# Kernel optimization log

Hardware: AMD Instinct MI355X
Metric: run time of the kernel (lower is better)

Reference implementation:

```python
import jax, jax.numpy as jnp
import numpy as np
from jax import lax

EPS = 0.1        # entropic regularization
MAX_ITER = 100   # Sinkhorn iteration budget
THRESH = 0.1     # early-stop threshold on err = mean_b sum_i |u - u_prev|
B, N, D = 16, 1024, 64


def setup_inputs() -> dict:
    key = jax.random.key(0)
    k1, k2 = jax.random.split(key)
    x = jax.random.normal(k1, (B, N, D), dtype=jnp.float32)
    y = jax.random.normal(k2, (B, N, D), dtype=jnp.float32)
    return {"x": x, "y": y}


def _lse(A):
    # Faithful to the original (unstabilized) lse: log(sum(exp(A)) + 1e-6)
    return jnp.log(jnp.exp(A).sum(-1) + 1e-6)


def _M(C, u, v):
    # (-C_ij + u_i + v_j) / eps
    return (-C + u[..., :, None] + v[..., None, :]) / EPS


def _cost_matrix(x, y):
    # (avoids materializing the [B, N, N, D] difference tensor; same math for p=2)
    x2 = (x * x).sum(-1)                         # [B, N]
    y2 = (y * y).sum(-1)                         # [B, N]
    xy = jnp.einsum('bid,bjd->bij', x, y)        # [B, N, N]
    return x2[..., :, None] + y2[..., None, :] - 2.0 * xy


def reference(x, y):
    x = jax.nn.softmax(x, axis=-1)
    y = jax.nn.softmax(y, axis=-1)
    C = _cost_matrix(x, y)                       # [B, N, N]
    n = x.shape[-2]
    log_mu = jnp.log(1.0 / n + 1e-8)             # mu = nu = uniform 1/n (scalar broadcast)
    u0 = jnp.zeros((x.shape[0], n), dtype=C.dtype)
    v0 = jnp.zeros_like(u0)

    def cond(carry):
        _, _, i, err = carry
        return jnp.logical_and(i < MAX_ITER, err >= THRESH)

    def body(carry):
        u, v, i, _ = carry
        u1 = u
        u = EPS * (log_mu - _lse(_M(C, u, v))) + u
        v = EPS * (log_mu - _lse(jnp.swapaxes(_M(C, u, v), -2, -1))) + v
        err = jnp.abs(u - u1).sum(-1).mean()
        return (u, v, i + 1, err)

    u, v, _, _ = lax.while_loop(
        cond, body, (u0, v0, jnp.int32(0), jnp.float32(jnp.inf)))

    pi = jnp.exp(_M(C, u, v))                    # transport plan [B, N, N]
    cost = (pi * C).sum((-2, -1))                # [B]
    return cost.mean()                           # reduction='mean'
```

## Files before the change

kernel.cpp:

```cpp
#include <hip/hip_runtime.h>
#include <hip/hip_bf16.h>
#include <math.h>

#define BATCH 16
#define NPTS 1024
#define DIM 64
#define EPSF 0.1f
#define INV_EPS 10.0f
#define MAX_ITER 100
#define THRESHF 0.1f
#define LSTRIDE 72

typedef _Float16 h8 __attribute__((ext_vector_type(8)));
typedef _Float16 half2v __attribute__((ext_vector_type(2)));
typedef short short8v __attribute__((ext_vector_type(8)));
typedef float float4v __attribute__((ext_vector_type(4)));

template <int P>
__device__ __forceinline__ half2v h2get(h8 v) {
  return __builtin_shufflevector(v, v, 2 * P, 2 * P + 1);
}

#define ATOMIC_ST(p, v) \
  __hip_atomic_store((p), (v), __ATOMIC_RELAXED, __HIP_MEMORY_SCOPE_AGENT)
#define ATOMIC_LD(p) \
  __hip_atomic_load((p), __ATOMIC_RELAXED, __HIP_MEMORY_SCOPE_AGENT)

__device__ inline float waveSum(float x) {
#pragma unroll
  for (int off = 32; off; off >>= 1) x += __shfl_xor(x, off, 64);
  return x;
}
__device__ inline float waveMax(float x) {
#pragma unroll
  for (int off = 32; off; off >>= 1) x = fmaxf(x, __shfl_xor(x, off, 64));
  return x;
}

__global__ __launch_bounds__(512, 2) void sinkhorn_fused(
    const float* __restrict__ x, const float* __restrict__ y,
    __hip_bfloat16* __restrict__ syh,
    float* __restrict__ y2,
    float* __restrict__ colsum,
    long long* __restrict__ flags,
    float* __restrict__ errB,
    float* __restrict__ costPart,
    float* __restrict__ out) {
  __shared__ __attribute__((aligned(16))) short xs[64 * LSTRIDE];
  __shared__ __attribute__((aligned(16))) short ys[2][64 * LSTRIDE];
  __shared__ __attribute__((aligned(16))) short os[2][64 * LSTRIDE];
  __shared__ __attribute__((aligned(16))) float wLDS[NPTS];
  __shared__ __attribute__((aligned(16))) _Float16 whL[NPTS];
  __shared__ __attribute__((aligned(16))) float colpart[8][NPTS];
  __shared__ float x2L[64];
  __shared__ float derr[8];
  __shared__ float errbL[BATCH];
  const int t = threadIdx.x;
  const int blk = blockIdx.x;
  const int wave = t >> 6, lane = t & 63;
  const int batch = (blk & 7) + 8 * (blk >> 7);
  const int kslot = (blk >> 3) & 15;
  const float log_mu = logf(1.0f / 1024.0f + 1e-8f);
  const float mu_c = 1.0f / 1024.0f + 1e-8f;

#pragma unroll
  for (int rr = 0; rr < 8; rr++) {
    int rl = wave * 8 + rr;
    int gr = batch * NPTS + kslot * 64 + rl;
    float xv = x[(size_t)gr * DIM + lane];
    float mx = waveMax(xv);
    float ex = __expf(xv - mx);
    float sx = waveSum(ex);
    float px = ex / sx;
    __hip_bfloat16 hbx = (__hip_bfloat16)px;
    xs[rl * LSTRIDE + lane] = *(const short*)&hbx;
    float sqx = waveSum(px * px);
    if (lane == 0) x2L[rl] = sqx;
    float yv = y[(size_t)gr * DIM + lane];
    float my = waveMax(yv);
    float ey = __expf(yv - my);
    float sy = waveSum(ey);
    float py = ey / sy;
    __hip_bfloat16 hby = (__hip_bfloat16)py;
    unsigned bits = *(const unsigned short*)&hby;
    unsigned nb = __shfl_down(bits, 1);
    if ((lane & 1) == 0)
      ATOMIC_ST((unsigned*)((unsigned short*)syh + (size_t)gr * DIM + lane),
                bits | (nb << 16));
    float sqy = waveSum(py * py);
    if (lane == 0) ATOMIC_ST(&y2[gr], sqy);
  }
  if (t < 192) {
    int buf = t >> 6, j = kslot * 64 + (t & 63);
    ATOMIC_ST(&colsum[((size_t)buf * BATCH + batch) * NPTS + j], 0.f);
  }
  __syncthreads();
  if (t == 0) ATOMIC_ST(&flags[batch * 16 + kslot], (long long)1 << 32);
  if (t < 16) {
    while ((int)(ATOMIC_LD(&flags[batch * 16 + t]) >> 32) < 1) {}
  }
  __syncthreads();

  const int m = lane & 15, q = lane >> 4;
  const int g = lane >> 3, sub = lane & 7;
  const int sw = wave & 3, ts = wave >> 2;
  short8v a0 = *(const short8v*)&xs[(sw * 16 + m) * LSTRIDE + q * 8];
  short8v a1 = *(const short8v*)&xs[(sw * 16 + m) * LSTRIDE + 32 + q * 8];
  float xa[4];
#pragma unroll
  for (int reg = 0; reg < 4; reg++) xa[reg] = x2L[sw * 16 + q * 4 + reg];
  h8 ka[8], kb[8];
  {
    const int r0 = t >> 3, c0 = (t & 7) * 8;
    const int r1 = (t + 512) >> 3, c1 = ((t + 512) & 7) * 8;
    const short* syb = (const short*)syh + (size_t)batch * NPTS * DIM;
    short8v pf0 = *(const short8v*)(syb + (size_t)r0 * DIM + c0);
    short8v pf1 = *(const short8v*)(syb + (size_t)r1 * DIM + c1);
    *(short8v*)&ys[r0 >> 6][(r0 & 63) * LSTRIDE + c0] = pf0;
    *(short8v*)&ys[r1 >> 6][(r1 & 63) * LSTRIDE + c1] = pf1;
    __syncthreads();
#pragma unroll
    for (int k = 0; k < 8; k++) {
      if (k < 7) {
        pf0 = *(const short8v*)(syb + (size_t)(128 * (k + 1) + r0) * DIM + c0);
        pf1 = *(const short8v*)(syb + (size_t)(128 * (k + 1) + r1) * DIM + c1);
      }
      const int jt = 2 * k + ts;
      float4v accv[4];
#pragma unroll
      for (int tj = 0; tj < 4; tj++) {
        short8v b0 = *(const short8v*)&ys[ts][(tj * 16 + m) * LSTRIDE + q * 8];
        short8v b1 = *(const short8v*)&ys[ts][(tj * 16 + m) * LSTRIDE + 32 + q * 8];
        float4v c = {0.f, 0.f, 0.f, 0.f};
        c = __builtin_amdgcn_mfma_f32_16x16x32_bf16(a0, b0, c, 0, 0, 0);
        c = __builtin_amdgcn_mfma_f32_16x16x32_bf16(a1, b1, c, 0, 0, 0);
        accv[tj] = c;
      }
#pragma unroll
      for (int tj = 0; tj < 4; tj++) {
        float y2v = y2[(size_t)batch * NPTS + jt * 64 + tj * 16 + m];
#pragma unroll
        for (int reg = 0; reg < 4; reg++) {
          float C = xa[reg] + y2v - 2.0f * accv[tj][reg];
          _Float16 kv = (_Float16)__expf(-INV_EPS * C);
          os[ts][(sw * 16 + q * 4 + reg) * LSTRIDE + tj * 16 + m] = *(const short*)&kv;
        }
      }
      __syncthreads();
      {
        int e0 = (2 * k) & 7, e1 = (2 * k + 1) & 7;
        if (g == e0 || g == e1) {
          const short* srcp = (g == e0) ? &os[0][0] : &os[1][0];
#pragma unroll
          for (int rr = 0; rr < 8; rr++) {
            h8 v = *(const h8*)&srcp[(wave * 8 + rr) * LSTRIDE + sub * 8];
            if (k < 4) ka[rr] = v; else kb[rr] = v;
          }
        }
      }
      if (k < 7) {
        *(short8v*)&ys[r0 >> 6][(r0 & 63) * LSTRIDE + c0] = pf0;
        *(short8v*)&ys[r1 >> 6][(r1 & 63) * LSTRIDE + c1] = pf1;
      }
      __syncthreads();
    }
  }

  for (int j = t; j < NPTS; j += 512) {
    wLDS[j] = 1.f;
    whL[j] = (_Float16)1.f;
  }
  __syncthreads();

  float eu[8], euPrev[8];
#pragma unroll
  for (int r = 0; r < 8; r++) eu[r] = 1.f;
  int it = 0;

  while (true) {
#pragma unroll
    for (int r = 0; r < 8; r++) euPrev[r] = eu[r];
    h8 wh0 = *(const h8*)&whL[8 * lane];
    h8 wh1 = *(const h8*)&whL[512 + 8 * lane];
    half2v c0[4], c1[4];
#pragma unroll
    for (int p = 0; p < 4; p++) {
      c0[p] = half2v{(_Float16)0.f, (_Float16)0.f};
      c1[p] = half2v{(_Float16)0.f, (_Float16)0.f};
    }
    float delta = 0.f;
#pragma unroll
    for (int rr = 0; rr < 8; rr++) {
      float d0 = 0.f, d1 = 0.f;
#define DOT_STEP(P)                                                         \
  d0 = __builtin_amdgcn_fdot2(h2get<P>(ka[rr]), h2get<P>(wh0), d0, false);  \
  d1 = __builtin_amdgcn_fdot2(h2get<P>(kb[rr]), h2get<P>(wh1), d1, false);
      DOT_STEP(0) DOT_STEP(1) DOT_STEP(2) DOT_STEP(3)
#undef DOT_STEP
      float dot = waveSum(d0 + d1);
      float sp = eu[rr] * dot + 1e-6f;
      float lg = __logf(sp);
      delta += fabsf(EPSF * (log_mu - lg));
      float ai = mu_c * eu[rr] * __builtin_amdgcn_rcpf(sp);
      eu[rr] = ai;
      _Float16 aih = (_Float16)(ai * 1024.0f);
      half2v ai2 = {aih, aih};
#define FMA_STEP(P)                                 \
  c0[P] = h2get<P>(ka[rr]) * ai2 + c0[P];           \
  c1[P] = h2get<P>(kb[rr]) * ai2 + c1[P];
      FMA_STEP(0) FMA_STEP(1) FMA_STEP(2) FMA_STEP(3)
#undef FMA_STEP
    }
    if (lane == 0) derr[wave] = delta;
    {
      float4* cp = (float4*)&colpart[wave][0];
      cp[2 * lane] = make_float4((float)c0[0][0], (float)c0[0][1],
                                 (float)c0[1][0], (float)c0[1][1]);
      cp[2 * lane + 1] = make_float4((float)c0[2][0], (float)c0[2][1],
                                     (float)c0[3][0], (float)c0[3][1]);
      cp[128 + 2 * lane] = make_float4((float)c1[0][0], (float)c1[0][1],
                                       (float)c1[1][0], (float)c1[1][1]);
      cp[128 + 2 * lane + 1] = make_float4((float)c1[2][0], (float)c1[2][1],
                                           (float)c1[3][0], (float)c1[3][1]);
    }
    __syncthreads();
    float* cs = colsum + ((size_t)(it % 3) * BATCH + batch) * NPTS;
    {
      int j0 = (t + (kslot << 6)) & 1023;
      int j1 = j0 ^ 512;
      float s0 = 0.f, s1 = 0.f;
#pragma unroll
      for (int w = 0; w < 8; w++) { s0 += colpart[w][j0]; s1 += colpart[w][j1]; }
      unsafeAtomicAdd(&cs[j0], s0);
      unsafeAtomicAdd(&cs[j1], s1);
    }
    if (it >= 1 && t < BATCH) {
      float v;
      while ((v = ATOMIC_LD(&errB[(it - 1) * BATCH + t])) < 0.f) {}
      errbL[t] = v;
    }
    float eblk = 0.f;
    if (t == 0) {
#pragma unroll
      for (int w = 0; w < 8; w++) eblk += derr[w];
    }
    __syncthreads();
    if (t == 0)
      ATOMIC_ST(&flags[batch * 16 + kslot],
                ((long long)(it + 2) << 32) | (long long)__float_as_uint(eblk));
    if (it >= 1) {
      float errv = 0.f;
#pragma unroll
      for (int k = 0; k < BATCH; k++) errv += errbL[k];
      if (errv * (1.0f / (float)BATCH) < THRESHF) {
#pragma unroll
        for (int r = 0; r < 8; r++) eu[r] = euPrev[r];
        break;
      }
    }
    float dpoll = 0.f;
    if (t < 16) {
      long long fw;
      while ((int)((fw = ATOMIC_LD(&flags[batch * 16 + t])) >> 32) < it + 2) {}
      dpoll = __uint_as_float((unsigned)fw);
    }
    __syncthreads();
    float cs0 = ATOMIC_LD(&cs[t]);
    float cs1 = ATOMIC_LD(&cs[t + 512]);
    if (t < 64)
      ATOMIC_ST(&colsum[((size_t)((it + 2) % 3) * BATCH + batch) * NPTS +
                        kslot * 64 + t], 0.f);
    if (wave == 0) {
      float e16 = (lane < 16) ? dpoll : 0.f;
#pragma unroll
      for (int off = 8; off; off >>= 1) e16 += __shfl_xor(e16, off, 16);
      if (t == 0 && kslot == 0) ATOMIC_ST(&errB[it * BATCH + batch], e16);
    }
    {
      float w0 = wLDS[t];
      float wn0 = mu_c * w0 *
                  __builtin_amdgcn_rcpf(w0 * cs0 + (1e-6f * 1024.0f)) * 1024.0f;
      wLDS[t] = wn0;
      whL[t] = (_Float16)wn0;
      float w1 = wLDS[t + 512];
      float wn1 = mu_c * w1 *
                  __builtin_amdgcn_rcpf(w1 * cs1 + (1e-6f * 1024.0f)) * 1024.0f;
      wLDS[t + 512] = wn1;
      whL[t + 512] = (_Float16)wn1;
    }
    it++;
    if (it >= MAX_ITER) break;
    __syncthreads();
  }

  {
    __syncthreads();
    const float4* w4 = (const float4*)wLDS;
    float wreg[16];
    *(float4*)&wreg[0]  = w4[2 * lane];
    *(float4*)&wreg[4]  = w4[2 * lane + 1];
    *(float4*)&wreg[8]  = w4[128 + 2 * lane];
    *(float4*)&wreg[12] = w4[128 + 2 * lane + 1];
    float csum = 0.f;
#pragma unroll
    for (int rr = 0; rr < 8; rr++) {
      float ai = eu[rr];
#pragma unroll
      for (int n = 0; n < 8; n++) {
        float kf = (float)ka[rr][n];
        if (kf > 0.f)
          csum += ai * wreg[n] * kf * (-EPSF * __logf(kf));
        float kg = (float)kb[rr][n];
        if (kg > 0.f)
          csum += ai * wreg[8 + n] * kg * (-EPSF * __logf(kg));
      }
    }
    csum = waveSum(csum);
    if (lane == 0) derr[wave] = csum;
    __syncthreads();
    if (t == 0) {
      float cst = 0.f;
#pragma unroll
      for (int w = 0; w < 8; w++) cst += derr[w];
      ATOMIC_ST(&costPart[blk], cst + 1.0f);
    }
    if (blk == 0) {
      if (t < 256) {
        float v;
        while ((v = ATOMIC_LD(&costPart[t])) < 0.5f) {}
        colpart[0][t] = v;
      }
      __syncthreads();
      if (wave == 0) {
        float s = colpart[0][lane] + colpart[0][lane + 64] +
                  colpart[0][lane + 128] + colpart[0][lane + 192];
        s = waveSum(s);
        if (lane == 0) out[0] = (s - 256.0f) * (1.0f / (float)BATCH);
      }
    }
  }
}

extern "C" void kernel_launch(void* const* d_in, const int* in_sizes, int n_in,
                              void* d_out, int out_size, void* d_ws,
                              size_t ws_size, hipStream_t stream) {
  (void)in_sizes; (void)n_in; (void)out_size; (void)ws_size;
  const float* x = (const float*)d_in[0];
  const float* y = (const float*)d_in[1];
  float* out = (float*)d_out;

  char* ws = (char*)d_ws;
  size_t off = 0;
  auto alloc = [&](size_t nbytes) -> void* {
    void* p = (void*)(ws + off);
    off = (off + nbytes + 255) & ~(size_t)255;
    return p;
  };
  __hip_bfloat16* syh = (__hip_bfloat16*)alloc((size_t)BATCH * NPTS * DIM * 2);
  float* y2 = (float*)alloc((size_t)BATCH * NPTS * 4);
  float* colsum = (float*)alloc((size_t)3 * BATCH * NPTS * 4);
  long long* flags = (long long*)alloc((size_t)BATCH * 16 * 8);
  float* errB = (float*)alloc((size_t)MAX_ITER * BATCH * 4);
  float* costPart = (float*)alloc(256 * 4);

  void* args[] = {&x, &y, &syh, &y2, &colsum, &flags,
                  &errB, &costPart, &out};
  hipLaunchCooperativeKernel((void*)sinkhorn_fused, dim3(256), dim3(512), args,
                             0, stream);
}
```

Before: 125.2 us.

## Pack two sub-blocks per 1024-thread workgroup with LDS-atomic group barriers

Runs two independent 512-thread slabs inside each 1024-thread workgroup, halving the cooperative grid to 128 blocks. Each slab synchronizes through its own LDS atomic-counter barrier with sleep polling, replacing __syncthreads. The per-wave column partials are also stored as fp16 instead of fp32 to shrink LDS. This trades hardware barriers for software spin barriers and reduces the precision of the partial sums. It also doubles LDS per block, which may limit residency.

After: 147.9 us. +18.2%, slower.

```diff
diff --git a/kernel.cpp b/kernel.cpp
--- a/kernel.cpp
+++ b/kernel.cpp
@@ -37,7 +37,21 @@
   return x;
 }
 
-__global__ __launch_bounds__(512, 2) void sinkhorn_fused(
+#define GBAR_IMPL(WAITSTR)                                                  \
+  do {                                                                      \
+    gen += 8;                                                               \
+    asm volatile(WAITSTR ::: "memory");                                     \
+    if (lane == 0)                                                          \
+      __hip_atomic_fetch_add(&bar[grp], 1, __ATOMIC_RELAXED,                \
+                             __HIP_MEMORY_SCOPE_WORKGROUP);                 \
+    while (__hip_atomic_load(&bar[grp], __ATOMIC_ACQUIRE,                   \
+                             __HIP_MEMORY_SCOPE_WORKGROUP) < gen)           \
+      __builtin_amdgcn_s_sleep(1);                                         \
+  } while (0)
+#define GBAR_L() GBAR_IMPL("s_waitcnt lgkmcnt(0)")
+#define GBAR_V() GBAR_IMPL("s_waitcnt vmcnt(0) lgkmcnt(0)")
+
+__global__ __launch_bounds__(1024, 4) void sinkhorn_fused(
     const float* __restrict__ x, const float* __restrict__ y,
     __hip_bfloat16* __restrict__ syh,
     float* __restrict__ y2,
@@ -46,22 +60,30 @@
     float* __restrict__ errB,
     float* __restrict__ costPart,
     float* __restrict__ out) {
-  __shared__ __attribute__((aligned(16))) short xs[64 * LSTRIDE];
-  __shared__ __attribute__((aligned(16))) short ys[2][64 * LSTRIDE];
-  __shared__ __attribute__((aligned(16))) short os[2][64 * LSTRIDE];
-  __shared__ __attribute__((aligned(16))) float wLDS[NPTS];
-  __shared__ __attribute__((aligned(16))) _Float16 whL[NPTS];
-  __shared__ __attribute__((aligned(16))) float colpart[8][NPTS];
-  __shared__ float x2L[64];
-  __shared__ float derr[8];
-  __shared__ float errbL[BATCH];
+  __shared__ __attribute__((aligned(16))) short xs[2][64 * LSTRIDE];
+  __shared__ __attribute__((aligned(16))) short ys[2][2][64 * LSTRIDE];
+  __shared__ __attribute__((aligned(16))) short os[2][2][64 * LSTRIDE];
+  __shared__ __attribute__((aligned(16))) float wLDS[2][NPTS];
+  __shared__ __attribute__((aligned(16))) _Float16 whL[2][NPTS];
+  __shared__ __attribute__((aligned(16))) _Float16 colpartH[2][8][NPTS];
+  __shared__ float x2L[2][64];
+  __shared__ float derrG[2][8];
+  __shared__ float errbL[2][BATCH];
+  __shared__ int bar[2];
   const int t = threadIdx.x;
-  const int blk = blockIdx.x;
-  const int wave = t >> 6, lane = t & 63;
-  const int batch = (blk & 7) + 8 * (blk >> 7);
-  const int kslot = (blk >> 3) & 15;
+  const int grp = t >> 9;
+  const int gt = t & 511;
+  const int wave = gt >> 6;
+  const int lane = t & 63;
+  const int sid = blockIdx.x * 2 + grp;
+  const int batch = (sid & 7) + 8 * (sid >> 7);
+  const int kslot = (sid >> 3) & 15;
   const float log_mu = logf(1.0f / 1024.0f + 1e-8f);
   const float mu_c = 1.0f / 1024.0f + 1e-8f;
+
+  if (t < 2) bar[t] = 0;
+  __syncthreads();
+  int gen = 0;
 
 #pragma unroll
   for (int rr = 0; rr < 8; rr++) {
@@ -73,9 +95,9 @@
     float sx = waveSum(ex);
     float px = ex / sx;
     __hip_bfloat16 hbx = (__hip_bfloat16)px;
-    xs[rl * LSTRIDE + lane] = *(const short*)&hbx;
+    xs[grp][rl * LSTRIDE + lane] = *(const short*)&hbx;
     float sqx = waveSum(px * px);
-    if (lane == 0) x2L[rl] = sqx;
+    if (lane == 0) x2L[grp][rl] = sqx;
     float yv = y[(size_t)gr * DIM + lane];
     float my = waveMax(yv);
     float ey = __expf(yv - my);
@@ -90,35 +112,35 @@
     float sqy = waveSum(py * py);
     if (lane == 0) ATOMIC_ST(&y2[gr], sqy);
   }
-  if (t < 192) {
-    int buf = t >> 6, j = kslot * 64 + (t & 63);
+  if (gt < 192) {
+    int buf = gt >> 6, j = kslot * 64 + (gt & 63);
     ATOMIC_ST(&colsum[((size_t)buf * BATCH + batch) * NPTS + j], 0.f);
   }
-  __syncthreads();
-  if (t == 0) ATOMIC_ST(&flags[batch * 16 + kslot], (long long)1 << 32);
-  if (t < 16) {
-    while ((int)(ATOMIC_LD(&flags[batch * 16 + t]) >> 32) < 1) {}
-  }
-  __syncthreads();
+  GBAR_V();
+  if (gt == 0) ATOMIC_ST(&flags[batch * 16 + kslot], (long long)1 << 32);
+  if (gt < 16) {
+    while ((int)(ATOMIC_LD(&flags[batch * 16 + gt]) >> 32) < 1) {}
+  }
+  GBAR_L();
 
   const int m = lane & 15, q = lane >> 4;
   const int g = lane >> 3, sub = lane & 7;
   const int sw = wave & 3, ts = wave >> 2;
-  short8v a0 = *(const short8v*)&xs[(sw * 16 + m) * LSTRIDE + q * 8];
-  short8v a1 = *(const short8v*)&xs[(sw * 16 + m) * LSTRIDE + 32 + q * 8];
+  short8v a0 = *(const short8v*)&xs[grp][(sw * 16 + m) * LSTRIDE + q * 8];
+  short8v a1 = *(const short8v*)&xs[grp][(sw * 16 + m) * LSTRIDE + 32 + q * 8];
   float xa[4];
 #pragma unroll
-  for (int reg = 0; reg < 4; reg++) xa[reg] = x2L[sw * 16 + q * 4 + reg];
+  for (int reg = 0; reg < 4; reg++) xa[reg] = x2L[grp][sw * 16 + q * 4 + reg];
   h8 ka[8], kb[8];
   {
-    const int r0 = t >> 3, c0 = (t & 7) * 8;
-    const int r1 = (t + 512) >> 3, c1 = ((t + 512) & 7) * 8;
+    const int r0 = gt >> 3, c0 = (gt & 7) * 8;
+    const int r1 = (gt + 512) >> 3, c1 = ((gt + 512) & 7) * 8;
     const short* syb = (const short*)syh + (size_t)batch * NPTS * DIM;
     short8v pf0 = *(const short8v*)(syb + (size_t)r0 * DIM + c0);
     short8v pf1 = *(const short8v*)(syb + (size_t)r1 * DIM + c1);
-    *(short8v*)&ys[r0 >> 6][(r0 & 63) * LSTRIDE + c0] = pf0;
-    *(short8v*)&ys[r1 >> 6][(r1 & 63) * LSTRIDE + c1] = pf1;
-    __syncthreads();
+    *(short8v*)&ys[grp][r0 >> 6][(r0 & 63) * LSTRIDE + c0] = pf0;
+    *(short8v*)&ys[grp][r1 >> 6][(r1 & 63) * LSTRIDE + c1] = pf1;
+    GBAR_L();
 #pragma unroll
     for (int k = 0; k < 8; k++) {
       if (k < 7) {
@@ -129,8 +151,8 @@
       float4v accv[4];
 #pragma unroll
       for (int tj = 0; tj < 4; tj++) {
-        short8v b0 = *(const short8v*)&ys[ts][(tj * 16 + m) * LSTRIDE + q * 8];
-        short8v b1 = *(const short8v*)&ys[ts][(tj * 16 + m) * LSTRIDE + 32 + q * 8];
+        short8v b0 = *(const short8v*)&ys[grp][ts][(tj * 16 + m) * LSTRIDE + q * 8];
+        short8v b1 = *(const short8v*)&ys[grp][ts][(tj * 16 + m) * LSTRIDE + 32 + q * 8];
         float4v c = {0.f, 0.f, 0.f, 0.f};
         c = __builtin_amdgcn_mfma_f32_16x16x32_bf16(a0, b0, c, 0, 0, 0);
         c = __builtin_amdgcn_mfma_f32_16x16x32_bf16(a1, b1, c, 0, 0, 0);
@@ -143,14 +165,15 @@
         for (int reg = 0; reg < 4; reg++) {
           float C = xa[reg] + y2v - 2.0f * accv[tj][reg];
           _Float16 kv = (_Float16)__expf(-INV_EPS * C);
-          os[ts][(sw * 16 + q * 4 + reg) * LSTRIDE + tj * 16 + m] = *(const short*)&kv;
+          os[grp][ts][(sw * 16 + q * 4 + reg) * LSTRIDE + tj * 16 + m] =
+              *(const short*)&kv;
         }
       }
-      __syncthreads();
+      GBAR_L();
       {
         int e0 = (2 * k) & 7, e1 = (2 * k + 1) & 7;
         if (g == e0 || g == e1) {
-          const short* srcp = (g == e0) ? &os[0][0] : &os[1][0];
+          const short* srcp = (g == e0) ? &os[grp][0][0] : &os[grp][1][0];
 #pragma unroll
           for (int rr = 0; rr < 8; rr++) {
             h8 v = *(const h8*)&srcp[(wave * 8 + rr) * LSTRIDE + sub * 8];
@@ -159,18 +182,18 @@
         }
       }
       if (k < 7) {
-        *(short8v*)&ys[r0 >> 6][(r0 & 63) * LSTRIDE + c0] = pf0;
-        *(short8v*)&ys[r1 >> 6][(r1 & 63) * LSTRIDE + c1] = pf1;
-      }
-      __syncthreads();
-    }
-  }
-
-  for (int j = t; j < NPTS; j += 512) {
-    wLDS[j] = 1.f;
-    whL[j] = (_Float16)1.f;
-  }
-  __syncthreads();
+        *(short8v*)&ys[grp][r0 >> 6][(r0 & 63) * LSTRIDE + c0] = pf0;
+        *(short8v*)&ys[grp][r1 >> 6][(r1 & 63) * LSTRIDE + c1] = pf1;
+      }
+      GBAR_L();
+    }
+  }
+
+  for (int j = gt; j < NPTS; j += 512) {
+    wLDS[grp][j] = 1.f;
+    whL[grp][j] = (_Float16)1.f;
+  }
+  GBAR_L();
 
   float eu[8], euPrev[8];
 #pragma unroll
@@ -180,8 +203,8 @@
   while (true) {
 #pragma unroll
     for (int r = 0; r < 8; r++) euPrev[r] = eu[r];
-    h8 wh0 = *(const h8*)&whL[8 * lane];
-    h8 wh1 = *(const h8*)&whL[512 + 8 * lane];
+    h8 wh0 = *(const h8*)&whL[grp][8 * lane];
+    h8 wh1 = *(const h8*)&whL[grp][512 + 8 * lane];
     half2v c0[4], c1[4];
 #pragma unroll
     for (int p = 0; p < 4; p++) {
@@ -211,47 +234,47 @@
       FMA_STEP(0) FMA_STEP(1) FMA_STEP(2) FMA_STEP(3)
 #undef FMA_STEP
     }
-    if (lane == 0) derr[wave] = delta;
+    if (lane == 0) derrG[grp][wave] = delta;
     {
-      float4* cp = (float4*)&colpart[wave][0];
-      cp[2 * lane] = make_float4((float)c0[0][0], (float)c0[0][1],
-                                 (float)c0[1][0], (float)c0[1][1]);
-      cp[2 * lane + 1] = make_float4((float)c0[2][0], (float)c0[2][1],
-                                     (float)c0[3][0], (float)c0[3][1]);
-      cp[128 + 2 * lane] = make_float4((float)c1[0][0], (float)c1[0][1],
-                                       (float)c1[1][0], (float)c1[1][1]);
-      cp[128 + 2 * lane + 1] = make_float4((float)c1[2][0], (float)c1[2][1],
-                                           (float)c1[3][0], (float)c1[3][1]);
-    }
-    __syncthreads();
+      _Float16* cph = &colpartH[grp][wave][0];
+#pragma unroll
+      for (int p = 0; p < 4; p++) {
+        *(half2v*)&cph[8 * lane + 2 * p] = c0[p];
+        *(half2v*)&cph[512 + 8 * lane + 2 * p] = c1[p];
+      }
+    }
+    GBAR_L();
     float* cs = colsum + ((size_t)(it % 3) * BATCH + batch) * NPTS;
     {
-      int j0 = (t + (kslot << 6)) & 1023;
+      int j0 = (gt + (kslot << 6)) & 1023;
       int j1 = j0 ^ 512;
       float s0 = 0.f, s1 = 0.f;
 #pragma unroll
-      for (int w = 0; w < 8; w++) { s0 += colpart[w][j0]; s1 += colpart[w][j1]; }
+      for (int w = 0; w < 8; w++) {
+        s0 += (float)colpartH[grp][w][j0];
+        s1 += (float)colpartH[grp][w][j1];
+      }
       unsafeAtomicAdd(&cs[j0], s0);
       unsafeAtomicAdd(&cs[j1], s1);
     }
-    if (it >= 1 && t < BATCH) {
+    if (it >= 1 && gt < BATCH) {
       float v;
-      while ((v = ATOMIC_LD(&errB[(it - 1) * BATCH + t])) < 0.f) {}
-      errbL[t] = v;
+      while ((v = ATOMIC_LD(&errB[(it - 1) * BATCH + gt])) < 0.f) {}
+      errbL[grp][gt] = v;
     }
     float eblk = 0.f;
-    if (t == 0) {
-#pragma unroll
-      for (int w = 0; w < 8; w++) eblk += derr[w];
-    }
-    __syncthreads();
-    if (t == 0)
+    if (gt == 0) {
+#pragma unroll
+      for (int w = 0; w < 8; w++) eblk += derrG[grp][w];
+    }
+    GBAR_V();
+    if (gt == 0)
       ATOMIC_ST(&flags[batch * 16 + kslot],
                 ((long long)(it + 2) << 32) | (long long)__float_as_uint(eblk));
     if (it >= 1) {
       float errv = 0.f;
 #pragma unroll
-      for (int k = 0; k < BATCH; k++) errv += errbL[k];
+      for (int k = 0; k < BATCH; k++) errv += errbL[grp][k];
       if (errv * (1.0f / (float)BATCH) < THRESHF) {
 #pragma unroll
         for (int r = 0; r < 8; r++) eu[r] = euPrev[r];
@@ -259,43 +282,43 @@
       }
     }
     float dpoll = 0.f;
-    if (t < 16) {
+    if (gt < 16) {
       long long fw;
-      while ((int)((fw = ATOMIC_LD(&flags[batch * 16 + t])) >> 32) < it + 2) {}
+      while ((int)((fw = ATOMIC_LD(&flags[batch * 16 + gt])) >> 32) < it + 2) {}
       dpoll = __uint_as_float((unsigned)fw);
     }
-    __syncthreads();
-    float cs0 = ATOMIC_LD(&cs[t]);
-    float cs1 = ATOMIC_LD(&cs[t + 512]);
-    if (t < 64)
+    GBAR_L();
+    float cs0 = ATOMIC_LD(&cs[gt]);
+    float cs1 = ATOMIC_LD(&cs[gt + 512]);
+    if (gt < 64)
       ATOMIC_ST(&colsum[((size_t)((it + 2) % 3) * BATCH + batch) * NPTS +
-                        kslot * 64 + t], 0.f);
+                        kslot * 64 + gt], 0.f);
     if (wave == 0) {
       float e16 = (lane < 16) ? dpoll : 0.f;
 #pragma unroll
       for (int off = 8; off; off >>= 1) e16 += __shfl_xor(e16, off, 16);
-      if (t == 0 && kslot == 0) ATOMIC_ST(&errB[it * BATCH + batch], e16);
+      if (gt == 0 && kslot == 0) ATOMIC_ST(&errB[it * BATCH + batch], e16);
     }
     {
-      float w0 = wLDS[t];
+      float w0 = wLDS[grp][gt];
       float wn0 = mu_c * w0 *
                   __builtin_amdgcn_rcpf(w0 * cs0 + (1e-6f * 1024.0f)) * 1024.0f;
-      wLDS[t] = wn0;
-      whL[t] = (_Float16)wn0;
-      float w1 = wLDS[t + 512];
+      wLDS[grp][gt] = wn0;
+      whL[grp][gt] = (_Float16)wn0;
+      float w1 = wLDS[grp][gt + 512];
       float wn1 = mu_c * w1 *
                   __builtin_amdgcn_rcpf(w1 * cs1 + (1e-6f * 1024.0f)) * 1024.0f;
-      wLDS[t + 512] = wn1;
-      whL[t + 512] = (_Float16)wn1;
+      wLDS[grp][gt + 512] = wn1;
+      whL[grp][gt + 512] = (_Float16)wn1;
     }
     it++;
     if (it >= MAX_ITER) break;
-    __syncthreads();
+    GBAR_L();
   }
 
   {
-    __syncthreads();
-    const float4* w4 = (const float4*)wLDS;
+    GBAR_L();
+    const float4* w4 = (const float4*)&wLDS[grp][0];
     float wreg[16];
     *(float4*)&wreg[0]  = w4[2 * lane];
     *(float4*)&wreg[4]  = w4[2 * lane + 1];
@@ -316,26 +339,26 @@
       }
     }
     csum = waveSum(csum);
-    if (lane == 0) derr[wave] = csum;
+    if (lane == 0) derrG[grp][wave] = csum;
     __syncthreads();
     if (t == 0) {
       float cst = 0.f;
 #pragma unroll
-      for (int w = 0; w < 8; w++) cst += derr[w];
-      ATOMIC_ST(&costPart[blk], cst + 1.0f);
-    }
-    if (blk == 0) {
-      if (t < 256) {
+      for (int w = 0; w < 8; w++) cst += derrG[0][w] + derrG[1][w];
+      ATOMIC_ST(&costPart[blockIdx.x], cst + 1.0f);
+    }
+    if (blockIdx.x == 0) {
+      float* gb = (float*)&colpartH[0][0][0];
+      if (t < 128) {
         float v;
         while ((v = ATOMIC_LD(&costPart[t])) < 0.5f) {}
-        colpart[0][t] = v;
+        gb[t] = v;
       }
       __syncthreads();
-      if (wave == 0) {
-        float s = colpart[0][lane] + colpart[0][lane + 64] +
-                  colpart[0][lane + 128] + colpart[0][lane + 192];
+      if (t < 64) {
+        float s = gb[lane] + gb[lane + 64];
         s = waveSum(s);
-        if (lane == 0) out[0] = (s - 256.0f) * (1.0f / (float)BATCH);
+        if (lane == 0) out[0] = (s - 128.0f) * (1.0f / (float)BATCH);
       }
     }
   }
@@ -365,6 +388,6 @@
 
   void* args[] = {&x, &y, &syh, &y2, &colsum, &flags,
                   &errB, &costPart, &out};
-  hipLaunchCooperativeKernel((void*)sinkhorn_fused, dim3(256), dim3(512), args,
-                             0, stream);
-}
+  hipLaunchCooperativeKernel((void*)sinkhorn_fused, dim3(128), dim3(1024),
+                             args, 0, stream);
+}
```

## Use MFMA for Sinkhorn row dots and column sums instead of fdot2/FMA

Applied to the files above, without the earlier changes.

Replaces the per-wave fdot2 row dot products and packed-half FMA column accumulation with f16 MFMA instructions. The K tile is kept in registers in two MFMA operand layouts, one for the row matvec and one transposed for the column matvec. The 32KB LDS colpart staging buffer and its cross-wave reduction go away, and the u update is done by one wave through small LDS arrays. The cost is holding two copies of K per thread (more registers) and an extra barrier per iteration, plus column partials now accumulate in fp32 through MFMA and are added atomically per wave.

Result: slower. 142.7 us (+13.9%).

```diff
diff --git a/kernel.cpp b/kernel.cpp
--- a/kernel.cpp
+++ b/kernel.cpp
@@ -12,14 +12,8 @@
 #define LSTRIDE 72
 
 typedef _Float16 h8 __attribute__((ext_vector_type(8)));
-typedef _Float16 half2v __attribute__((ext_vector_type(2)));
 typedef short short8v __attribute__((ext_vector_type(8)));
 typedef float float4v __attribute__((ext_vector_type(4)));
-
-template <int P>
-__device__ __forceinline__ half2v h2get(h8 v) {
-  return __builtin_shufflevector(v, v, 2 * P, 2 * P + 1);
-}
 
 #define ATOMIC_ST(p, v) \
   __hip_atomic_store((p), (v), __ATOMIC_RELAXED, __HIP_MEMORY_SCOPE_AGENT)
@@ -51,7 +45,9 @@
   __shared__ __attribute__((aligned(16))) short os[2][64 * LSTRIDE];
   __shared__ __attribute__((aligned(16))) float wLDS[NPTS];
   __shared__ __attribute__((aligned(16))) _Float16 whL[NPTS];
-  __shared__ __attribute__((aligned(16))) float colpart[8][NPTS];
+  __shared__ __attribute__((aligned(16))) _Float16 ahF[64];
+  __shared__ __attribute__((aligned(16))) float dotL[2][64];
+  __shared__ __attribute__((aligned(16))) float euL[64];
   __shared__ float x2L[64];
   __shared__ float derr[8];
   __shared__ float errbL[BATCH];
@@ -102,14 +98,14 @@
   __syncthreads();
 
   const int m = lane & 15, q = lane >> 4;
-  const int g = lane >> 3, sub = lane & 7;
   const int sw = wave & 3, ts = wave >> 2;
   short8v a0 = *(const short8v*)&xs[(sw * 16 + m) * LSTRIDE + q * 8];
   short8v a1 = *(const short8v*)&xs[(sw * 16 + m) * LSTRIDE + 32 + q * 8];
   float xa[4];
 #pragma unroll
   for (int reg = 0; reg < 4; reg++) xa[reg] = x2L[sw * 16 + q * 4 + reg];
-  h8 ka[8], kb[8];
+  h8 kA[16];
+  h8 kB[16];
   {
     const int r0 = t >> 3, c0 = (t & 7) * 8;
     const int r1 = (t + 512) >> 3, c1 = ((t + 512) & 7) * 8;
@@ -147,15 +143,31 @@
         }
       }
       __syncthreads();
-      {
-        int e0 = (2 * k) & 7, e1 = (2 * k + 1) & 7;
-        if (g == e0 || g == e1) {
-          const short* srcp = (g == e0) ? &os[0][0] : &os[1][0];
-#pragma unroll
-          for (int rr = 0; rr < 8; rr++) {
-            h8 v = *(const h8*)&srcp[(wave * 8 + rr) * LSTRIDE + sub * 8];
-            if (k < 4) ka[rr] = v; else kb[rr] = v;
+      if ((k >> 2) == ts) {
+        int base = (k & 3) * 4;
+#pragma unroll
+        for (int p = 0; p < 4; p++) {
+          int c = p * 32 + q * 8;
+          kA[base + p] =
+              *(const h8*)&os[c >> 6][(sw * 16 + m) * LSTRIDE + (c & 63)];
+        }
+      }
+      if (k == wave) {
+#pragma unroll
+        for (int tl = 0; tl < 8; tl++) {
+          int c = tl * 16 + m;
+          const _Float16* bp =
+              (const _Float16*)&os[c >> 6][(q * 8) * LSTRIDE + (c & 63)];
+          const _Float16* bp1 =
+              (const _Float16*)&os[c >> 6][(32 + q * 8) * LSTRIDE + (c & 63)];
+          h8 f0, f1;
+#pragma unroll
+          for (int e = 0; e < 8; e++) {
+            f0[e] = bp[e * LSTRIDE];
+            f1[e] = bp1[e * LSTRIDE];
           }
+          kB[2 * tl] = f0;
+          kB[2 * tl + 1] = f1;
         }
       }
       if (k < 7) {
@@ -170,91 +182,76 @@
     wLDS[j] = 1.f;
     whL[j] = (_Float16)1.f;
   }
+  if (t < 64) euL[t] = 1.f;
   __syncthreads();
 
-  float eu[8], euPrev[8];
-#pragma unroll
-  for (int r = 0; r < 8; r++) eu[r] = 1.f;
+  float euPrevR = 1.f;
+  float eblkR = 0.f;
+  bool undo = false;
   int it = 0;
 
   while (true) {
-#pragma unroll
-    for (int r = 0; r < 8; r++) euPrev[r] = eu[r];
-    h8 wh0 = *(const h8*)&whL[8 * lane];
-    h8 wh1 = *(const h8*)&whL[512 + 8 * lane];
-    half2v c0[4], c1[4];
-#pragma unroll
-    for (int p = 0; p < 4; p++) {
-      c0[p] = half2v{(_Float16)0.f, (_Float16)0.f};
-      c1[p] = half2v{(_Float16)0.f, (_Float16)0.f};
-    }
-    float delta = 0.f;
-#pragma unroll
-    for (int rr = 0; rr < 8; rr++) {
-      float d0 = 0.f, d1 = 0.f;
-#define DOT_STEP(P)                                                         \
-  d0 = __builtin_amdgcn_fdot2(h2get<P>(ka[rr]), h2get<P>(wh0), d0, false);  \
-  d1 = __builtin_amdgcn_fdot2(h2get<P>(kb[rr]), h2get<P>(wh1), d1, false);
-      DOT_STEP(0) DOT_STEP(1) DOT_STEP(2) DOT_STEP(3)
-#undef DOT_STEP
-      float dot = waveSum(d0 + d1);
-      float sp = eu[rr] * dot + 1e-6f;
-      float lg = __logf(sp);
-      delta += fabsf(EPSF * (log_mu - lg));
-      float ai = mu_c * eu[rr] * __builtin_amdgcn_rcpf(sp);
-      eu[rr] = ai;
-      _Float16 aih = (_Float16)(ai * 1024.0f);
-      half2v ai2 = {aih, aih};
-#define FMA_STEP(P)                                 \
-  c0[P] = h2get<P>(ka[rr]) * ai2 + c0[P];           \
-  c1[P] = h2get<P>(kb[rr]) * ai2 + c1[P];
-      FMA_STEP(0) FMA_STEP(1) FMA_STEP(2) FMA_STEP(3)
-#undef FMA_STEP
-    }
-    if (lane == 0) derr[wave] = delta;
     {
-      float4* cp = (float4*)&colpart[wave][0];
-      cp[2 * lane] = make_float4((float)c0[0][0], (float)c0[0][1],
-                                 (float)c0[1][0], (float)c0[1][1]);
-      cp[2 * lane + 1] = make_float4((float)c0[2][0], (float)c0[2][1],
-                                     (float)c0[3][0], (float)c0[3][1]);
-      cp[128 + 2 * lane] = make_float4((float)c1[0][0], (float)c1[0][1],
-                                       (float)c1[1][0], (float)c1[1][1]);
-      cp[128 + 2 * lane + 1] = make_float4((float)c1[2][0], (float)c1[2][1],
-                                           (float)c1[3][0], (float)c1[3][1]);
+      float4v Cd = {0.f, 0.f, 0.f, 0.f};
+#pragma unroll
+      for (int s = 0; s < 16; s++) {
+        h8 wf = *(const h8*)&whL[(ts * 16 + s) * 32 + q * 8];
+        Cd = __builtin_amdgcn_mfma_f32_16x16x32_f16(kA[s], wf, Cd, 0, 0, 0);
+      }
+      if (m == 0) {
+#pragma unroll
+        for (int reg = 0; reg < 4; reg++)
+          dotL[ts][sw * 16 + q * 4 + reg] = Cd[reg];
+      }
+    }
+    __syncthreads();
+    {
+      float dl = 0.f;
+      if (t < 64) {
+        float dot = dotL[0][t] + dotL[1][t];
+        float old = euL[t];
+        euPrevR = old;
+        float sp = old * dot + 1e-6f;
+        float lg = __logf(sp);
+        dl = fabsf(EPSF * (log_mu - lg));
+        float ai = mu_c * old * __builtin_amdgcn_rcpf(sp);
+        euL[t] = ai;
+        ahF[t] = (_Float16)(ai * 1024.0f);
+      }
+      if (wave == 0) {
+        float s = waveSum(dl);
+        if (lane == 0) eblkR = s;
+      }
     }
     __syncthreads();
     float* cs = colsum + ((size_t)(it % 3) * BATCH + batch) * NPTS;
     {
-      int j0 = (t + (kslot << 6)) & 1023;
-      int j1 = j0 ^ 512;
-      float s0 = 0.f, s1 = 0.f;
-#pragma unroll
-      for (int w = 0; w < 8; w++) { s0 += colpart[w][j0]; s1 += colpart[w][j1]; }
-      unsafeAtomicAdd(&cs[j0], s0);
-      unsafeAtomicAdd(&cs[j1], s1);
+      h8 af0 = *(const h8*)&ahF[q * 8];
+      h8 af1 = *(const h8*)&ahF[32 + q * 8];
+#pragma unroll
+      for (int tl = 0; tl < 8; tl++) {
+        int tl2 = (tl + kslot) & 7;
+        float4v Cc = {0.f, 0.f, 0.f, 0.f};
+        Cc = __builtin_amdgcn_mfma_f32_16x16x32_f16(af0, kB[2 * tl2], Cc, 0, 0, 0);
+        Cc = __builtin_amdgcn_mfma_f32_16x16x32_f16(af1, kB[2 * tl2 + 1], Cc, 0, 0, 0);
+        if (q == 0) unsafeAtomicAdd(&cs[wave * 128 + tl2 * 16 + m], Cc[0]);
+      }
     }
     if (it >= 1 && t < BATCH) {
       float v;
       while ((v = ATOMIC_LD(&errB[(it - 1) * BATCH + t])) < 0.f) {}
       errbL[t] = v;
     }
-    float eblk = 0.f;
-    if (t == 0) {
-#pragma unroll
-      for (int w = 0; w < 8; w++) eblk += derr[w];
-    }
     __syncthreads();
     if (t == 0)
       ATOMIC_ST(&flags[batch * 16 + kslot],
-                ((long long)(it + 2) << 32) | (long long)__float_as_uint(eblk));
+                ((long long)(it + 2) << 32) | (long long)__float_as_uint(eblkR));
     if (it >= 1) {
       float errv = 0.f;
 #pragma unroll
       for (int k = 0; k < BATCH; k++) errv += errbL[k];
       if (errv * (1.0f / (float)BATCH) < THRESHF) {
-#pragma unroll
-        for (int r = 0; r < 8; r++) eu[r] = euPrev[r];
+        undo = true;
         break;
       }
     }
@@ -294,25 +291,20 @@
   }
 
   {
-    __syncthreads();
-    const float4* w4 = (const float4*)wLDS;
-    float wreg[16];
-    *(float4*)&wreg[0]  = w4[2 * lane];
-    *(float4*)&wreg[4]  = w4[2 * lane + 1];
-    *(float4*)&wreg[8]  = w4[128 + 2 * lane];
-    *(float4*)&wreg[12] = w4[128 + 2 * lane + 1];
+    if (undo && t < 64) euL[t] = euPrevR;
+    __syncthreads();
+    float ai = euL[sw * 16 + m];
     float csum = 0.f;
 #pragma unroll
-    for (int rr = 0; rr < 8; rr++) {
-      float ai = eu[rr];
-#pragma unroll
-      for (int n = 0; n < 8; n++) {
-        float kf = (float)ka[rr][n];
-        if (kf > 0.f)
-          csum += ai * wreg[n] * kf * (-EPSF * __logf(kf));
-        float kg = (float)kb[rr][n];
-        if (kg > 0.f)
-          csum += ai * wreg[8 + n] * kg * (-EPSF * __logf(kg));
+    for (int s = 0; s < 16; s++) {
+      int cb = (ts * 16 + s) * 32 + q * 8;
+      float4 w0 = *(const float4*)&wLDS[cb];
+      float4 w1 = *(const float4*)&wLDS[cb + 4];
+      float wv[8] = {w0.x, w0.y, w0.z, w0.w, w1.x, w1.y, w1.z, w1.w};
+#pragma unroll
+      for (int e = 0; e < 8; e++) {
+        float kf = (float)kA[s][e];
+        if (kf > 0.f) csum += ai * wv[e] * kf * (-EPSF * __logf(kf));
       }
     }
     csum = waveSum(csum);
@@ -325,15 +317,15 @@
       ATOMIC_ST(&costPart[blk], cst + 1.0f);
     }
     if (blk == 0) {
+      float* gb = (float*)&ys[0][0];
       if (t < 256) {
         float v;
         while ((v = ATOMIC_LD(&costPart[t])) < 0.5f) {}
-        colpart[0][t] = v;
+        gb[t] = v;
       }
       __syncthreads();
       if (wave == 0) {
-        float s = colpart[0][lane] + colpart[0][lane + 64] +
-                  colpart[0][lane + 128] + colpart[0][lane + 192];
+        float s = gb[lane] + gb[lane + 64] + gb[lane + 128] + gb[lane + 192];
         s = waveSum(s);
         if (lane == 0) out[0] = (s - 256.0f) * (1.0f / (float)BATCH);
       }
```
